# Optimization experiments

Hardware: AMD Instinct MI355X
Metric: run time of the kernel (lower is better)

## Reference

```python
import jax, jax.numpy as jnp
import numpy as np

D_MODEL = 1024
N_HEADS = 8
HEAD_DIM = D_MODEL // N_HEADS
B, T = 4, 2048


def setup_inputs() -> dict:
    key = jax.random.key(0)
    ks = jax.random.split(key, 10)
    x = jax.random.normal(ks[0], (B, T, D_MODEL), dtype=jnp.float32)
    # causal mask: True entries are masked (matches torch masked_fill semantics)
    mask = jnp.triu(jnp.ones((T, T), dtype=bool), k=1)

    def xavier(k, shape):
        fan_in, fan_out = shape[1], shape[0]
        lim = float(np.sqrt(6.0 / (fan_in + fan_out)))
        return jax.random.uniform(k, shape, jnp.float32, -lim, lim)

    Wq = xavier(ks[1], (D_MODEL, D_MODEL)); bq = jnp.zeros((D_MODEL,), jnp.float32)
    Wk = xavier(ks[2], (D_MODEL, D_MODEL)); bk = jnp.zeros((D_MODEL,), jnp.float32)
    Wv = xavier(ks[3], (D_MODEL, D_MODEL)); bv = jnp.zeros((D_MODEL,), jnp.float32)
    Wo = xavier(ks[4], (D_MODEL, D_MODEL)); bo = jnp.zeros((D_MODEL,), jnp.float32)
    return {"x": x, "mask": mask, "Wq": Wq, "bq": bq, "Wk": Wk, "bk": bk,
            "Wv": Wv, "bv": bv, "Wo": Wo, "bo": bo}


def reference(x, mask, Wq, bq, Wk, bk, Wv, bv, Wo, bo):
    Bsz, Tlen, _ = x.shape
    # torch Linear: y = x @ W.T + b
    Q = (x @ Wq.T + bq).reshape(Bsz, Tlen, N_HEADS, HEAD_DIM).transpose(0, 2, 1, 3)  # [B,H,T,Dh]
    K = (x @ Wk.T + bk).reshape(Bsz, Tlen, N_HEADS, HEAD_DIM).transpose(0, 2, 1, 3)  # [B,H,T,Dh]
    V_shared = x @ Wv.T + bv  # [B,T,D] shared across heads
    scale = 1.0 / jnp.sqrt(jnp.float32(HEAD_DIM))
    scores = jnp.einsum('bhqd,bhkd->bhqk', Q, K) * scale  # [B,H,T,T]
    scores = jnp.where(mask[None, None, :, :], jnp.float32(-1e9), scores)
    attn_per_head = jax.nn.softmax(scores, axis=-1)
    alpha_agg = attn_per_head.mean(axis=1)  # [B,T,T] head-averaged attention
    out = jnp.einsum('bqk,bkd->bqd', alpha_agg, V_shared) @ Wo.T + bo
    return out, alpha_agg
```

## Files before the change

### kernel.cpp

```cpp
#include <hip/hip_runtime.h>
#include <hip/hip_bf16.h>

#define D_MODEL 1024
#define NH 8
#define HD 128
#define BATCH 4
#define TSEQ 2048
#define MROWS (BATCH * TSEQ)
#define QKV_LD 3072
#define SBAND 131072
#define SBATCH ((size_t)SBAND * 136)

typedef __attribute__((ext_vector_type(8))) __bf16 bf16x8;
typedef __attribute__((ext_vector_type(4))) __bf16 bf16x4;
typedef __attribute__((ext_vector_type(4))) float f32x4;
typedef __attribute__((ext_vector_type(8))) unsigned short u16x8;

#define SC2 0.1275174441680632f

__device__ __forceinline__ void gload16(const void* g, void* lds) {
  __builtin_amdgcn_global_load_lds(
      (const __attribute__((address_space(1))) unsigned int*)g,
      (__attribute__((address_space(3))) unsigned int*)lds, 16, 0, 0);
}

__device__ __forceinline__ dim3 swz_grid() {
  const int nx = gridDim.x, ny = gridDim.y;
  const int nwg = nx * ny * gridDim.z;
  int L = blockIdx.x + nx * (blockIdx.y + ny * blockIdx.z);
  const int q = nwg >> 3, r = nwg & 7;
  const int xcd = L & 7, idx = L >> 3;
  int t = (xcd < r ? xcd * (q + 1) : r * (q + 1) + (xcd - r) * q) + idx;
  dim3 o;
  o.x = t % nx; t /= nx;
  o.y = t % ny;
  o.z = t / ny;
  return o;
}

__global__ __launch_bounds__(256) void cvt_f32_to_bf16(const float* __restrict__ in,
                                                       __bf16* __restrict__ out, int n4) {
  int i = blockIdx.x * 256 + threadIdx.x;
  if (i < n4) {
    float4 v = reinterpret_cast<const float4*>(in)[i];
    bf16x4 o;
    o[0] = (__bf16)v.x; o[1] = (__bf16)v.y; o[2] = (__bf16)v.z; o[3] = (__bf16)v.w;
    reinterpret_cast<bf16x4*>(out)[i] = o;
  }
}

__global__ __launch_bounds__(256) void cvt4_weights(const float* __restrict__ w0,
                                                    const float* __restrict__ w1,
                                                    const float* __restrict__ w2,
                                                    const float* __restrict__ w3,
                                                    __bf16* __restrict__ out) {
  const int per = D_MODEL * D_MODEL / 4;
  int i = blockIdx.x * 256 + threadIdx.x;
  int m = i / per, j = i - m * per;
  const float* src = (m == 0) ? w0 : (m == 1) ? w1 : (m == 2) ? w2 : w3;
  float4 v = reinterpret_cast<const float4*>(src)[j];
  bf16x4 o;
  o[0] = (__bf16)v.x; o[1] = (__bf16)v.y; o[2] = (__bf16)v.z; o[3] = (__bf16)v.w;
  reinterpret_cast<bf16x4*>(out)[i] = o;
}

__global__ __launch_bounds__(256) void concat_bias(const float* __restrict__ a,
                                                   const float* __restrict__ b,
                                                   const float* __restrict__ c,
                                                   float* __restrict__ o) {
  int i = blockIdx.x * 256 + threadIdx.x;
  if (i < 3072) o[i] = (i < 1024) ? a[i] : (i < 2048) ? b[i - 1024] : c[i - 2048];
}

template <bool BF16OUT, bool CAUSAL, bool AFP32>
__global__ __launch_bounds__(256) void gemm128(const void* __restrict__ Aip,
                                               const __bf16* __restrict__ Bp,
                                               const float* __restrict__ bias,
                                               void* __restrict__ Yp, int K, int ldy,
                                               size_t sA, size_t sB, size_t sY) {
  __shared__ __bf16 sm[16384];
  __bf16* const As0 = sm;
  __bf16* const Bs0 = sm + 8192;
  const dim3 bi = swz_grid();
  const int tid = threadIdx.x;
  const int w = tid >> 6, l = tid & 63;
  const int lr = l & 15, lg = l >> 4;
  const int m0 = bi.y * 128, n0 = bi.x * 128;
  const int z = bi.z;
  const __bf16* Ab = AFP32 ? nullptr : (const __bf16*)Aip + z * sA;
  const float* Af = AFP32 ? (const float*)Aip + z * sA : nullptr;
  const __bf16* Bb = Bp + z * sB;
  const int wm = w >> 1, wn = w & 1;
  f32x4 acc[4][4] = {};
  const int Klim = CAUSAL ? (m0 + 128 < K ? m0 + 128 : K) : K;
  const int nt = Klim >> 5;

  auto stage = [&](int t, int buf) {
    const int k0 = t << 5;
    __bf16* As = As0 + buf * 4096;
    __bf16* Bs = Bs0 + buf * 4096;
    if constexpr (!AFP32) {
#pragma unroll
      for (int i = 0; i < 2; ++i) {
        int s = w * 128 + i * 64 + l;
        int row = s >> 2, scp = s & 3;
        int sc = scp ^ ((row >> 1) & 3);
        gload16(Ab + (size_t)(m0 + row) * K + k0 + sc * 8, (char*)As + s * 16);
      }
    } else {
#pragma unroll
      for (int i = 0; i < 2; ++i) {
        int s = w * 128 + i * 64 + l;
        int row = s >> 2, sc = s & 3;
        const float* src = Af + (size_t)(m0 + row) * K + k0 + sc * 8;
        float4 lo = *reinterpret_cast<const float4*>(src);
        float4 hi = *reinterpret_cast<const float4*>(src + 4);
        bf16x8 v;
        v[0] = (__bf16)lo.x; v[1] = (__bf16)lo.y; v[2] = (__bf16)lo.z; v[3] = (__bf16)lo.w;
        v[4] = (__bf16)hi.x; v[5] = (__bf16)hi.y; v[6] = (__bf16)hi.z; v[7] = (__bf16)hi.w;
        int p = row * 4 + (sc ^ ((row >> 1) & 3));
        *reinterpret_cast<bf16x8*>((char*)As + p * 16) = v;
      }
    }
#pragma unroll
    for (int i = 0; i < 2; ++i) {
      int s = w * 128 + i * 64 + l;
      int row = s >> 2, scp = s & 3;
      int sc = scp ^ ((row >> 1) & 3);
      gload16(Bb + (size_t)(n0 + row) * K + k0 + sc * 8, (char*)Bs + s * 16);
    }
  };

  stage(0, 0);
  __syncthreads();
  int cur = 0;
  for (int t = 0; t < nt; ++t) {
    if (t + 1 < nt) stage(t + 1, cur ^ 1);
    bf16x8 af[4], bf[4];
#pragma unroll
    for (int f = 0; f < 4; ++f) {
      int ar = wm * 64 + f * 16 + lr;
      af[f] = *reinterpret_cast<const bf16x8*>((const char*)(As0 + cur * 4096) + ar * 64 +
                                               ((lg ^ ((ar >> 1) & 3)) * 16));
      int br = wn * 64 + f * 16 + lr;
      bf[f] = *reinterpret_cast<const bf16x8*>((const char*)(Bs0 + cur * 4096) + br * 64 +
                                               ((lg ^ ((br >> 1) & 3)) * 16));
    }
#pragma unroll
    for (int mf = 0; mf < 4; ++mf)
#pragma unroll
      for (int nf = 0; nf < 4; ++nf)
        acc[mf][nf] = __builtin_amdgcn_mfma_f32_16x16x32_bf16(af[mf], bf[nf], acc[mf][nf], 0, 0, 0);
    __syncthreads();
    cur ^= 1;
  }

  if constexpr (BF16OUT) {
    float bv[4];
#pragma unroll
    for (int nf = 0; nf < 4; ++nf) bv[nf] = bias ? bias[n0 + wn * 64 + nf * 16 + lr] : 0.f;
#pragma unroll
    for (int mf = 0; mf < 4; ++mf)
#pragma unroll
      for (int r = 0; r < 4; ++r) {
        int row = wm * 64 + mf * 16 + lg * 4 + r;
#pragma unroll
        for (int nf = 0; nf < 4; ++nf) {
          int col = wn * 64 + nf * 16 + lr;
          int pseg = (col >> 3) ^ (row & 15);
          sm[row * 128 + pseg * 8 + (col & 7)] = (__bf16)(acc[mf][nf][r] + bv[nf]);
        }
      }
    __syncthreads();
    __bf16* Yb = (__bf16*)Yp + z * sY;
#pragma unroll
    for (int i = 0; i < 8; ++i) {
      int s = i * 256 + tid;
      int row = s >> 4, pseg = s & 15;
      int lseg = pseg ^ (row & 15);
      bf16x8 v = *reinterpret_cast<bf16x8*>(sm + row * 128 + pseg * 8);
      *reinterpret_cast<bf16x8*>(&Yb[(size_t)(m0 + row) * ldy + n0 + lseg * 8]) = v;
    }
  } else {
#pragma unroll
    for (int mf = 0; mf < 4; ++mf)
#pragma unroll
      for (int nf = 0; nf < 4; ++nf)
#pragma unroll
        for (int r = 0; r < 4; ++r) {
          int grow = m0 + wm * 64 + mf * 16 + lg * 4 + r;
          int gcol = n0 + wn * 64 + nf * 16 + lr;
          float v = acc[mf][nf][r];
          if (bias) v += bias[gcol];
          ((float*)Yp + z * sY)[(size_t)grow * ldy + gcol] = v;
        }
  }
}

__global__ __launch_bounds__(256) void transpose_v(const __bf16* __restrict__ V,
                                                   __bf16* __restrict__ Vt) {
  __shared__ unsigned short tile[64 * 72];
  const int b = blockIdx.z;
  const int t0 = blockIdx.x * 64, d0 = blockIdx.y * 64;
  const int tid = threadIdx.x;
#pragma unroll
  for (int i = 0; i < 2; ++i) {
    int s = i * 256 + tid;
    int r = s >> 3, c8 = s & 7;
    u16x8 v = *reinterpret_cast<const u16x8*>(V + ((size_t)b * TSEQ + t0 + r) * QKV_LD + d0 + c8 * 8);
    *reinterpret_cast<u16x8*>(&tile[r * 72 + c8 * 8]) = v;
  }
  __syncthreads();
#pragma unroll
  for (int i = 0; i < 2; ++i) {
    int s = i * 256 + tid;
    int dr = s >> 3, t8 = s & 7;
    u16x8 o;
#pragma unroll
    for (int j = 0; j < 8; ++j) o[j] = tile[(t8 * 8 + j) * 72 + dr];
    *reinterpret_cast<u16x8*>(Vt + ((size_t)b * D_MODEL + d0 + dr) * TSEQ + t0 + t8 * 8) = o;
  }
}

__global__ __launch_bounds__(256) void score_gemm(const __bf16* __restrict__ QKV,
                                                  __bf16* __restrict__ S,
                                                  float* __restrict__ lsum,
                                                  int b0, size_t sstride) {
  __shared__ __bf16 sm[16384];
  __bf16* const As0 = sm;
  __bf16* const Bs0 = sm + 8192;
  const dim3 bi = swz_grid();
  const int tid = threadIdx.x;
  const int w = tid >> 6, l = tid & 63;
  const int lr = l & 15, lg = l >> 4;
  const int wm = w >> 1, wn = w & 1;
  const int idx = bi.x;
  const int h = bi.y;
  const int zz = bi.z;
  const int b = b0 + zz;
  int qt = (int)((sqrtf(8.f * (float)idx + 1.f) - 1.f) * 0.5f);
  while ((qt + 1) * (qt + 2) / 2 <= idx) ++qt;
  while (qt * (qt + 1) / 2 > idx) --qt;
  const int kt = idx - qt * (qt + 1) / 2;
  const int q0 = qt * 128, k0 = kt * 128;
  const int kext = (qt + 1) * 128;
  const bool diag = (kt == qt);

  const __bf16* Ab = QKV + (size_t)(b * TSEQ + q0) * QKV_LD + h * HD;
  const __bf16* Bb = QKV + (size_t)(b * TSEQ + k0) * QKV_LD + 1024 + h * HD;

  auto stage = [&](int t, int buf) {
    __bf16* As = As0 + buf * 4096;
    __bf16* Bs = Bs0 + buf * 4096;
#pragma unroll
    for (int i = 0; i < 2; ++i) {
      int s = w * 128 + i * 64 + l;
      int row = s >> 2, scp = s & 3;
      int sc = scp ^ ((row >> 1) & 3);
      gload16(Ab + (size_t)row * QKV_LD + t * 32 + sc * 8, (char*)As + s * 16);
    }
#pragma unroll
    for (int i = 0; i < 2; ++i) {
      int s = w * 128 + i * 64 + l;
      int row = s >> 2, scp = s & 3;
      int sc = scp ^ ((row >> 1) & 3);
      gload16(Bb + (size_t)row * QKV_LD + t * 32 + sc * 8, (char*)Bs + s * 16);
    }
  };

  f32x4 acc[4][4] = {};
  stage(0, 0);
  __syncthreads();
  int cur = 0;
#pragma unroll
  for (int t = 0; t < 4; ++t) {
    if (t < 3) stage(t + 1, cur ^ 1);
    bf16x8 af[4], bf[4];
#pragma unroll
    for (int f = 0; f < 4; ++f) {
      int ar = wm * 64 + f * 16 + lr;
      af[f] = *reinterpret_cast<const bf16x8*>((const char*)(As0 + cur * 4096) + ar * 64 +
                                               ((lg ^ ((ar >> 1) & 3)) * 16));
      int br = wn * 64 + f * 16 + lr;
      bf[f] = *reinterpret_cast<const bf16x8*>((const char*)(Bs0 + cur * 4096) + br * 64 +
                                               ((lg ^ ((br >> 1) & 3)) * 16));
    }
#pragma unroll
    for (int mf = 0; mf < 4; ++mf)
#pragma unroll
      for (int nf = 0; nf < 4; ++nf)
        acc[mf][nf] = __builtin_amdgcn_mfma_f32_16x16x32_bf16(af[mf], bf[nf], acc[mf][nf], 0, 0, 0);
    __syncthreads();
    cur ^= 1;
  }

  float ls[4][4] = {};
#pragma unroll
  for (int mf = 0; mf < 4; ++mf)
#pragma unroll
    for (int r = 0; r < 4; ++r) {
      int row = wm * 64 + mf * 16 + lg * 4 + r;
#pragma unroll
      for (int nf = 0; nf < 4; ++nf) {
        int col = wn * 64 + nf * 16 + lr;
        float ev = exp2f(acc[mf][nf][r] * SC2);
        int pseg = (col >> 3) ^ (row & 15);
        sm[row * 128 + pseg * 8 + (col & 7)] = (__bf16)ev;
        if (!diag || col <= row) ls[mf][r] += ev;
      }
    }
#pragma unroll
  for (int m = 1; m < 16; m <<= 1)
#pragma unroll
    for (int mf = 0; mf < 4; ++mf)
#pragma unroll
      for (int r = 0; r < 4; ++r) ls[mf][r] += __shfl_xor(ls[mf][r], m, 64);
  if (lr == 0) {
#pragma unroll
    for (int mf = 0; mf < 4; ++mf)
#pragma unroll
      for (int r = 0; r < 4; ++r)
        atomicAdd(&lsum[((size_t)(b * NH + h)) * TSEQ + q0 + wm * 64 + mf * 16 + lg * 4 + r],
                  ls[mf][r]);
  }
  __syncthreads();
  __bf16* Sb = S + zz * sstride + (size_t)SBAND * ((qt * (qt + 1)) >> 1) +
               (size_t)h * 128 * kext + k0;
#pragma unroll
  for (int i = 0; i < 8; ++i) {
    int s = i * 256 + tid;
    int row = s >> 4, pseg = s & 15;
    int lseg = pseg ^ (row & 15);
    bf16x8 v = *reinterpret_cast<bf16x8*>(sm + row * 128 + pseg * 8);
    *reinterpret_cast<bf16x8*>(&Sb[(size_t)row * kext + lseg * 8]) = v;
  }
}

__global__ __launch_bounds__(256) void alpha_stream(const __bf16* __restrict__ S,
                                                    const float* __restrict__ lsum,
                                                    float* __restrict__ alpha,
                                                    int b0, size_t sstride) {
  const int q = blockIdx.x;
  const int zz = blockIdx.y;
  const int b = b0 + zz;
  const int qt = q >> 7;
  const int kext = (qt + 1) * 128;
  const int k0 = threadIdx.x * 8;
  float* arow = alpha + ((size_t)(b * TSEQ + q)) * TSEQ + k0;
  if (k0 >= kext) {
    float4 zzf = {0.f, 0.f, 0.f, 0.f};
    *reinterpret_cast<float4*>(arow) = zzf;
    *reinterpret_cast<float4*>(arow + 4) = zzf;
    return;
  }
  const __bf16* Sb = S + zz * sstride + (size_t)SBAND * ((qt * (qt + 1)) >> 1) +
                     (size_t)(q & 127) * kext + k0;
  const size_t hstride = (size_t)128 * kext;
  float o[8] = {};
#pragma unroll
  for (int h = 0; h < NH; ++h) {
    float li = 1.0f / (8.0f * lsum[((size_t)(b * NH + h)) * TSEQ + q]);
    bf16x8 s8 = *reinterpret_cast<const bf16x8*>(Sb + h * hstride);
#pragma unroll
    for (int j = 0; j < 8; ++j) o[j] += (float)s8[j] * li;
  }
#pragma unroll
  for (int j = 0; j < 8; ++j)
    if (k0 + j > q) o[j] = 0.f;
  float4 lo = {o[0], o[1], o[2], o[3]};
  float4 hi = {o[4], o[5], o[6], o[7]};
  *reinterpret_cast<float4*>(arow) = lo;
  *reinterpret_cast<float4*>(arow + 4) = hi;
}

extern "C" void kernel_launch(void* const* d_in, const int* in_sizes, int n_in,
                              void* d_out, int out_size, void* d_ws, size_t ws_size,
                              hipStream_t stream) {
  const float* x  = (const float*)d_in[0];
  const float* Wq = (const float*)d_in[2];
  const float* bq = (const float*)d_in[3];
  const float* Wk = (const float*)d_in[4];
  const float* bk = (const float*)d_in[5];
  const float* Wv = (const float*)d_in[6];
  const float* bv = (const float*)d_in[7];
  const float* Wo = (const float*)d_in[8];
  const float* bo = (const float*)d_in[9];

  float* out_f = (float*)d_out;
  float* alpha = out_f + (size_t)MROWS * D_MODEL;

  char* p = (char*)d_ws;
  __bf16* xb   = (__bf16*)p; p += (size_t)MROWS * D_MODEL * 2;
  __bf16* wqb  = (__bf16*)p; p += (size_t)D_MODEL * D_MODEL * 2;
  __bf16* wkb  = (__bf16*)p; p += (size_t)D_MODEL * D_MODEL * 2;
  __bf16* wvb  = (__bf16*)p; p += (size_t)D_MODEL * D_MODEL * 2;
  __bf16* wob  = (__bf16*)p; p += (size_t)D_MODEL * D_MODEL * 2;
  __bf16* qkv  = (__bf16*)p; p += (size_t)MROWS * QKV_LD * 2;
  __bf16* vtb  = (__bf16*)p; p += (size_t)BATCH * D_MODEL * TSEQ * 2;
  float* lsum  = (float*)p;  p += (size_t)BATCH * NH * TSEQ * 4;
  float* bcat  = (float*)p;  p += 3072 * 4;
  __bf16* sbuf = (__bf16*)p;
  __bf16* midb = xb;

  size_t used = (size_t)((char*)sbuf - (char*)d_ws);
  size_t sb1 = SBATCH * 2;
  int NB = 1;
  if (ws_size >= used + 4 * sb1) NB = 4;
  else if (ws_size >= used + 2 * sb1) NB = 2;
  size_t sstride = (NB > 1) ? SBATCH : 0;

  hipMemsetAsync(lsum, 0, (size_t)BATCH * NH * TSEQ * 4, stream);

  {
    int n4 = MROWS * D_MODEL / 4;
    cvt_f32_to_bf16<<<n4 / 256, 256, 0, stream>>>(x, xb, n4);
    int w4 = 4 * D_MODEL * D_MODEL / 4;
    cvt4_weights<<<w4 / 256, 256, 0, stream>>>(Wq, Wk, Wv, Wo, wqb);
    concat_bias<<<12, 256, 0, stream>>>(bq, bk, bv, bcat);
  }

  gemm128<true, false, false><<<dim3(QKV_LD / 128, MROWS / 128), 256, 0, stream>>>(
      xb, wqb, bcat, qkv, D_MODEL, QKV_LD, 0, 0, 0);

  transpose_v<<<dim3(TSEQ / 64, D_MODEL / 64, BATCH), 256, 0, stream>>>(qkv + 2048, vtb);

  for (int b0 = 0; b0 < BATCH; b0 += NB) {
    score_gemm<<<dim3(136, NH, NB), 256, 0, stream>>>(qkv, sbuf, lsum, b0, sstride);
    alpha_stream<<<dim3(TSEQ, NB), 256, 0, stream>>>(sbuf, lsum, alpha, b0, sstride);
  }

  gemm128<true, true, true><<<dim3(D_MODEL / 128, TSEQ / 128, BATCH), 256, 0, stream>>>(
      alpha, vtb, nullptr, midb, TSEQ, D_MODEL,
      (size_t)TSEQ * TSEQ, (size_t)D_MODEL * TSEQ, (size_t)TSEQ * D_MODEL);

  gemm128<false, false, false><<<dim3(D_MODEL / 128, MROWS / 128), 256, 0, stream>>>(
      midb, wob, bo, out_f, D_MODEL, D_MODEL, 0, 0, 0);
}
```

Baseline: 360.6 us.

## Loop over all heads inside each score_gemm block instead of one head per block

Each score_gemm block now walks all 8 heads sequentially over a 32-step K loop, writing exp-scores and row sums after every 4 steps. The grid shrinks by a factor of 8, so the number of launched blocks drops sharply. The LDS-staged coalesced store is replaced with direct scattered 2-byte global stores. This cuts per-block launch and prologue overhead but greatly reduces parallelism and makes the S writes uncoalesced, which can hurt both occupancy and memory efficiency.

```diff
diff --git a/kernel.cpp b/kernel.cpp
--- a/kernel.cpp
+++ b/kernel.cpp
@@ -235,8 +235,7 @@
   const int lr = l & 15, lg = l >> 4;
   const int wm = w >> 1, wn = w & 1;
   const int idx = bi.x;
-  const int h = bi.y;
-  const int zz = bi.z;
+  const int zz = bi.y;
   const int b = b0 + zz;
   int qt = (int)((sqrtf(8.f * (float)idx + 1.f) - 1.f) * 0.5f);
   while ((qt + 1) * (qt + 2) / 2 <= idx) ++qt;
@@ -246,10 +245,11 @@
   const int kext = (qt + 1) * 128;
   const bool diag = (kt == qt);
 
-  const __bf16* Ab = QKV + (size_t)(b * TSEQ + q0) * QKV_LD + h * HD;
-  const __bf16* Bb = QKV + (size_t)(b * TSEQ + k0) * QKV_LD + 1024 + h * HD;
+  const __bf16* Ab = QKV + (size_t)(b * TSEQ + q0) * QKV_LD;
+  const __bf16* Bb = QKV + (size_t)(b * TSEQ + k0) * QKV_LD + 1024;
 
   auto stage = [&](int t, int buf) {
+    const int kk = t << 5;
     __bf16* As = As0 + buf * 4096;
     __bf16* Bs = Bs0 + buf * 4096;
 #pragma unroll
@@ -257,14 +257,14 @@
       int s = w * 128 + i * 64 + l;
       int row = s >> 2, scp = s & 3;
       int sc = scp ^ ((row >> 1) & 3);
-      gload16(Ab + (size_t)row * QKV_LD + t * 32 + sc * 8, (char*)As + s * 16);
+      gload16(Ab + (size_t)row * QKV_LD + kk + sc * 8, (char*)As + s * 16);
     }
 #pragma unroll
     for (int i = 0; i < 2; ++i) {
       int s = w * 128 + i * 64 + l;
       int row = s >> 2, scp = s & 3;
       int sc = scp ^ ((row >> 1) & 3);
-      gload16(Bb + (size_t)row * QKV_LD + t * 32 + sc * 8, (char*)Bs + s * 16);
+      gload16(Bb + (size_t)row * QKV_LD + kk + sc * 8, (char*)Bs + s * 16);
     }
   };
 
@@ -272,9 +272,10 @@
   stage(0, 0);
   __syncthreads();
   int cur = 0;
-#pragma unroll
-  for (int t = 0; t < 4; ++t) {
-    if (t < 3) stage(t + 1, cur ^ 1);
+  __bf16* Sband = S + zz * sstride + (size_t)SBAND * ((qt * (qt + 1)) >> 1) + k0;
+#pragma unroll 1
+  for (int t = 0; t < 32; ++t) {
+    if (t < 31) stage(t + 1, cur ^ 1);
     bf16x8 af[4], bf[4];
 #pragma unroll
     for (int f = 0; f < 4; ++f) {
@@ -290,49 +291,43 @@
 #pragma unroll
       for (int nf = 0; nf < 4; ++nf)
         acc[mf][nf] = __builtin_amdgcn_mfma_f32_16x16x32_bf16(af[mf], bf[nf], acc[mf][nf], 0, 0, 0);
+
+    if ((t & 3) == 3) {
+      const int h = t >> 2;
+      __bf16* Sb = Sband + (size_t)h * 128 * kext;
+      float ls[4][4] = {};
+#pragma unroll
+      for (int mf = 0; mf < 4; ++mf)
+#pragma unroll
+        for (int r = 0; r < 4; ++r) {
+          int row = wm * 64 + mf * 16 + lg * 4 + r;
+          __bf16* srow = Sb + (size_t)row * kext;
+#pragma unroll
+          for (int nf = 0; nf < 4; ++nf) {
+            int col = wn * 64 + nf * 16 + lr;
+            float ev = exp2f(acc[mf][nf][r] * SC2);
+            srow[col] = (__bf16)ev;
+            if (!diag || col <= row) ls[mf][r] += ev;
+            acc[mf][nf][r] = 0.f;
+          }
+        }
+#pragma unroll
+      for (int m = 1; m < 16; m <<= 1)
+#pragma unroll
+        for (int mf = 0; mf < 4; ++mf)
+#pragma unroll
+          for (int r = 0; r < 4; ++r) ls[mf][r] += __shfl_xor(ls[mf][r], m, 64);
+      if (lr == 0) {
+#pragma unroll
+        for (int mf = 0; mf < 4; ++mf)
+#pragma unroll
+          for (int r = 0; r < 4; ++r)
+            atomicAdd(&lsum[((size_t)(b * NH + h)) * TSEQ + q0 + wm * 64 + mf * 16 + lg * 4 + r],
+                      ls[mf][r]);
+      }
+    }
     __syncthreads();
     cur ^= 1;
-  }
-
-  float ls[4][4] = {};
-#pragma unroll
-  for (int mf = 0; mf < 4; ++mf)
-#pragma unroll
-    for (int r = 0; r < 4; ++r) {
-      int row = wm * 64 + mf * 16 + lg * 4 + r;
-#pragma unroll
-      for (int nf = 0; nf < 4; ++nf) {
-        int col = wn * 64 + nf * 16 + lr;
-        float ev = exp2f(acc[mf][nf][r] * SC2);
-        int pseg = (col >> 3) ^ (row & 15);
-        sm[row * 128 + pseg * 8 + (col & 7)] = (__bf16)ev;
-        if (!diag || col <= row) ls[mf][r] += ev;
-      }
-    }
-#pragma unroll
-  for (int m = 1; m < 16; m <<= 1)
-#pragma unroll
-    for (int mf = 0; mf < 4; ++mf)
-#pragma unroll
-      for (int r = 0; r < 4; ++r) ls[mf][r] += __shfl_xor(ls[mf][r], m, 64);
-  if (lr == 0) {
-#pragma unroll
-    for (int mf = 0; mf < 4; ++mf)
-#pragma unroll
-      for (int r = 0; r < 4; ++r)
-        atomicAdd(&lsum[((size_t)(b * NH + h)) * TSEQ + q0 + wm * 64 + mf * 16 + lg * 4 + r],
-                  ls[mf][r]);
-  }
-  __syncthreads();
-  __bf16* Sb = S + zz * sstride + (size_t)SBAND * ((qt * (qt + 1)) >> 1) +
-               (size_t)h * 128 * kext + k0;
-#pragma unroll
-  for (int i = 0; i < 8; ++i) {
-    int s = i * 256 + tid;
-    int row = s >> 4, pseg = s & 15;
-    int lseg = pseg ^ (row & 15);
-    bf16x8 v = *reinterpret_cast<bf16x8*>(sm + row * 128 + pseg * 8);
-    *reinterpret_cast<bf16x8*>(&Sb[(size_t)row * kext + lseg * 8]) = v;
   }
 }
 
@@ -425,7 +420,7 @@
   transpose_v<<<dim3(TSEQ / 64, D_MODEL / 64, BATCH), 256, 0, stream>>>(qkv + 2048, vtb);
 
   for (int b0 = 0; b0 < BATCH; b0 += NB) {
-    score_gemm<<<dim3(136, NH, NB), 256, 0, stream>>>(qkv, sbuf, lsum, b0, sstride);
+    score_gemm<<<dim3(136, NB), 256, 0, stream>>>(qkv, sbuf, lsum, b0, sstride);
     alpha_stream<<<dim3(TSEQ, NB), 256, 0, stream>>>(sbuf, lsum, alpha, b0, sstride);
   }
 
```

Result: no change. 362.2 us (+0.5%).
